# Kernel optimization log

Measured on AMD Instinct MI355X. Metric: run time of the kernel, lower is better.

## Reference

```python
import jax, jax.numpy as jnp
import numpy as np

B, S, D = 8, 4096, 256
NUM_WINDOW = 8
WIN = S // NUM_WINDOW          # 512
H = 2                          # num_heads
K = D                          # key_dim = d_model per source
DFF = 1024
LN_EPS = 1e-3                  # keras LayerNormalization default epsilon


def _layer_norm(x, g, b):
    mu = jnp.mean(x, axis=-1, keepdims=True)
    var = jnp.mean(jnp.square(x - mu), axis=-1, keepdims=True)
    return (x - mu) * jax.lax.rsqrt(var + LN_EPS) * g + b


def setup_inputs() -> dict:
    key = jax.random.key(0)
    ks = jax.random.split(key, 12)
    s = 0.02
    inp = {
        "x": jax.random.normal(ks[0], (B, S, D), dtype=jnp.float32),
        # MHA projections (keras MultiHeadAttention layout)
        "Wq": jax.random.normal(ks[1], (D, H, K), dtype=jnp.float32) * s,
        "bq": jnp.zeros((H, K), dtype=jnp.float32),
        "Wk": jax.random.normal(ks[2], (D, H, K), dtype=jnp.float32) * s,
        "bk": jnp.zeros((H, K), dtype=jnp.float32),
        "Wv": jax.random.normal(ks[3], (D, H, K), dtype=jnp.float32) * s,
        "bv": jnp.zeros((H, K), dtype=jnp.float32),
        "Wo": jax.random.normal(ks[4], (H, K, D), dtype=jnp.float32) * s,
        "bo": jnp.zeros((D,), dtype=jnp.float32),
        "ln1_g": jnp.ones((D,), dtype=jnp.float32),
        "ln1_b": jnp.zeros((D,), dtype=jnp.float32),
        # FeedForward
        "W1": jax.random.normal(ks[5], (D, DFF), dtype=jnp.float32) * s,
        "b1": jnp.zeros((DFF,), dtype=jnp.float32),
        "W2": jax.random.normal(ks[6], (DFF, D), dtype=jnp.float32) * s,
        "b2": jnp.zeros((D,), dtype=jnp.float32),
        "ln2_g": jnp.ones((D,), dtype=jnp.float32),
        "ln2_b": jnp.zeros((D,), dtype=jnp.float32),
    }
    return inp


def reference(x, Wq, bq, Wk, bk, Wv, bv, Wo, bo, ln1_g, ln1_b,
              W1, b1, W2, b2, ln2_g, ln2_b):
    # --- Localized self-attention: block-diagonal over NUM_WINDOW windows ---
    xw = x.reshape(B, NUM_WINDOW, WIN, D)               # [b, w, s, d]
    q = jnp.einsum('bwsd,dhk->bwshk', xw, Wq) + bq      # [b, w, s, h, k]
    k = jnp.einsum('bwsd,dhk->bwshk', xw, Wk) + bk
    v = jnp.einsum('bwsd,dhk->bwshk', xw, Wv) + bv
    scores = jnp.einsum('bwshk,bwthk->bwhst', q, k) / jnp.sqrt(
        jnp.asarray(K, dtype=x.dtype))                  # [b, w, h, s, t]
    attn = jax.nn.softmax(scores, axis=-1)
    ctx = jnp.einsum('bwhst,bwthk->bwshk', attn, v)     # [b, w, s, h, k]
    attn_out = jnp.einsum('bwshk,hkd->bwsd', ctx, Wo) + bo
    attn_out = attn_out.reshape(B, S, D)                # concat over windows
    x = _layer_norm(x + attn_out, ln1_g, ln1_b)
    # --- FeedForward (dropout inactive at inference) ---
    h = jax.nn.relu(x @ W1 + b1)
    ff = h @ W2 + b2
    return _layer_norm(x + ff, ln2_g, ln2_b)
```

## Files before the change

kernel.cpp:

```cpp
#include <hip/hip_runtime.h>

typedef unsigned short u16;
typedef short short8 __attribute__((ext_vector_type(8)));
typedef float f32x4 __attribute__((ext_vector_type(4)));

#define AS1C const __attribute__((address_space(1))) void*
#define AS3P __attribute__((address_space(3))) void*

__device__ __forceinline__ u16 f2b(float f) {
  unsigned u = __float_as_uint(f);
  return (u16)((u + 0x7fffu + ((u >> 16) & 1u)) >> 16);
}
__device__ __forceinline__ float b2f(u16 h) {
  return __uint_as_float((unsigned)h << 16);
}

#define BB 8
#define SS 4096
#define DD 256
#define MTOK (BB*SS)

#define OFF_WQKVT  ((size_t)0)
#define OFF_WOT    ((size_t)786432)
#define OFF_W1T    ((size_t)1048576)
#define OFF_W2T    ((size_t)1572864)
#define OFF_BQKV   ((size_t)2097152)
#define OFF_XB     ((size_t)2103296)
#define OFF_QKV    ((size_t)18880512)
#define OFF_YB     ((size_t)52434944)
#define OFF_HB     ((size_t)69212160)
#define OFF_VT     ((size_t)119543808)
#define OFF_CTX    ((size_t)153098240)
#define OFF_S      ((size_t)186652672)

__global__ __launch_bounds__(256) void cast_x_kernel(const float* __restrict__ x,
                                                     u16* __restrict__ xb) {
  size_t i = ((size_t)blockIdx.x * 256 + threadIdx.x) * 4;
  float4 v = *(const float4*)(x + i);
  ushort4 o;
  o.x = f2b(v.x); o.y = f2b(v.y); o.z = f2b(v.z); o.w = f2b(v.w);
  *(ushort4*)(xb + i) = o;
}

__global__ __launch_bounds__(256) void prep_w_kernel(
    const float* __restrict__ Wq, const float* __restrict__ Wk, const float* __restrict__ Wv,
    const float* __restrict__ Wo, const float* __restrict__ W1, const float* __restrict__ W2,
    const float* __restrict__ bq, const float* __restrict__ bk, const float* __restrict__ bv,
    u16* __restrict__ wqkvt, u16* __restrict__ wot, u16* __restrict__ w1t,
    u16* __restrict__ w2t, float* __restrict__ bqkv)
{
  for (int i = blockIdx.x * 256 + threadIdx.x; i < 1050112; i += 1024 * 256) {
    if (i < 393216) {
      int n = i >> 8, d = i & 255;
      const float* W = (n < 512) ? Wq : (n < 1024) ? Wk : Wv;
      int nn = n & 511;
      wqkvt[i] = f2b(W[d * 512 + nn]);
    } else if (i < 524288) {
      int j = i - 393216;
      int dout = j >> 9, hk = j & 511;
      wot[j] = f2b(Wo[hk * 256 + dout]);
    } else if (i < 786432) {
      int j = i - 524288;
      int f = j >> 8, d = j & 255;
      w1t[j] = f2b(W1[d * 1024 + f]);
    } else if (i < 1048576) {
      int j = i - 786432;
      int d = j >> 10, f = j & 1023;
      w2t[j] = f2b(W2[f * 256 + d]);
    } else {
      int n = i - 1048576;
      bqkv[n] = (n < 512) ? bq[n] : (n < 1024) ? bk[n - 512] : bv[n - 1024];
    }
  }
}

__global__ __launch_bounds__(256) void gemm_nres(
    const u16* __restrict__ A, const u16* __restrict__ BT,
    const float* __restrict__ bias, u16* __restrict__ C,
    u16* __restrict__ vt, int N, int vbase, int relu)
{
  __shared__ __align__(16) u16 lds[32768];
  const int tid = threadIdx.x, lane = tid & 63, wid = tid >> 6;
  const int ln = lane & 15, quad = lane >> 4;
  const int pn = blockIdx.x >> 6;
  const int mg = blockIdx.x & 63;
  const int wm = (wid >> 1) << 5;
  const int wn = (wid & 1) << 6;
  const long mbase = (long)mg << 9;
  const int nb = pn << 7;
  const u16* Bp = BT + (size_t)nb * 256;
  const u16* Ap = A + (size_t)mbase * 256;

#pragma unroll
  for (int p = 0; p < 16; p++) {
    const int s = p * 256 + tid;
    const int row = s >> 5, pc = s & 31;
    const int c = pc ^ (row & 31);
    __builtin_amdgcn_global_load_lds(
        (AS1C)(Bp + (size_t)row * 256 + c * 8), (AS3P)(lds + s * 8), 16, 0, 0);
  }
  __syncthreads();
  short8 breg[4][8];
#pragma unroll
  for (int j = 0; j < 4; j++) {
    const int row = wn + j * 16 + ln;
#pragma unroll
    for (int ks = 0; ks < 8; ks++)
      breg[j][ks] = *(const short8*)(lds + row * 256 + (((ks << 2) + quad) ^ (row & 31)) * 8);
  }
  __syncthreads();

#pragma unroll
  for (int p = 0; p < 8; p++) {
    const int s = p * 256 + tid;
    const int row = s >> 5, pc = s & 31;
    const int c = pc ^ (row & 31);
    __builtin_amdgcn_global_load_lds(
        (AS1C)(Ap + (size_t)row * 256 + c * 8), (AS3P)(lds + s * 8), 16, 0, 0);
  }

  for (int it = 0; it < 8; it++) {
    const int cur = it & 1;
    const u16* Ab = lds + cur * 16384;
    __syncthreads();
    if (it + 1 < 8) {
      const u16* An = Ap + (size_t)(it + 1) * 64 * 256;
      u16* Ax = lds + (cur ^ 1) * 16384;
#pragma unroll
      for (int p = 0; p < 8; p++) {
        const int s = p * 256 + tid;
        const int row = s >> 5, pc = s & 31;
        const int c = pc ^ (row & 31);
        __builtin_amdgcn_global_load_lds(
            (AS1C)(An + (size_t)row * 256 + c * 8), (AS3P)(Ax + s * 8), 16, 0, 0);
      }
    }
    f32x4 acc[2][4];
#pragma unroll
    for (int i = 0; i < 2; i++)
#pragma unroll
      for (int j = 0; j < 4; j++) acc[i][j] = (f32x4){0.f, 0.f, 0.f, 0.f};
    const int r0 = wm + ln, r1 = wm + 16 + ln;
#pragma unroll
    for (int ks = 0; ks < 8; ks++) {
      const short8 a0 = *(const short8*)(Ab + r0 * 256 + (((ks << 2) + quad) ^ (r0 & 31)) * 8);
      const short8 a1 = *(const short8*)(Ab + r1 * 256 + (((ks << 2) + quad) ^ (r1 & 31)) * 8);
#pragma unroll
      for (int j = 0; j < 4; j++) {
        acc[0][j] = __builtin_amdgcn_mfma_f32_16x16x32_bf16(breg[j][ks], a0, acc[0][j], 0, 0, 0);
        acc[1][j] = __builtin_amdgcn_mfma_f32_16x16x32_bf16(breg[j][ks], a1, acc[1][j], 0, 0, 0);
      }
    }
    const long mrow0 = mbase + it * 64;
    if (nb < vbase) {
#pragma unroll
      for (int i = 0; i < 2; i++) {
        const long m = mrow0 + wm + i * 16 + ln;
#pragma unroll
        for (int j = 0; j < 4; j++) {
          const int n0 = nb + wn + j * 16 + quad * 4;
          f32x4 v = acc[i][j];
          const float4 b4 = *(const float4*)(bias + n0);
          v[0] += b4.x; v[1] += b4.y; v[2] += b4.z; v[3] += b4.w;
          if (relu) {
#pragma unroll
            for (int r = 0; r < 4; r++) v[r] = fmaxf(v[r], 0.f);
          }
          ushort4 ob;
          ob.x = f2b(v[0]); ob.y = f2b(v[1]); ob.z = f2b(v[2]); ob.w = f2b(v[3]);
          *(ushort4*)(C + (size_t)m * N + n0) = ob;
        }
      }
    } else {
#pragma unroll
      for (int i = 0; i < 2; i++) {
        const long m = mrow0 + wm + i * 16 + ln;
        const int bw = (int)(m >> 9), t = (int)(m & 511);
#pragma unroll
        for (int j = 0; j < 4; j++) {
          const int n0 = nb + wn + j * 16 + quad * 4;
          const int h = (n0 - vbase) >> 8, k0 = (n0 - vbase) & 255;
          u16* vp = vt + (size_t)(bw * 2 + h) * 131072 + (size_t)k0 * 512 + t;
          const float4 b4 = *(const float4*)(bias + n0);
          vp[0]    = f2b(acc[i][j][0] + b4.x);
          vp[512]  = f2b(acc[i][j][1] + b4.y);
          vp[1024] = f2b(acc[i][j][2] + b4.z);
          vp[1536] = f2b(acc[i][j][3] + b4.w);
        }
      }
    }
  }
}

__global__ __launch_bounds__(512) void bgemm_qk(const u16* __restrict__ qkv,
                                                u16* __restrict__ S)
{
  __shared__ __align__(16) u16 As[64 * 32];
  __shared__ __align__(16) u16 Bs[512 * 32];
  __shared__ float red1[8][64], red2[8][64];
  const int tid = threadIdx.x, lane = tid & 63, wid = tid >> 6;
  const int ln = lane & 15, quad = lane >> 4;
  const int bat = blockIdx.x & 127, mt = blockIdx.x >> 7;
  const int bw = bat >> 1, h = bat & 1;
  const u16* Qb = qkv + (size_t)bw * 786432 + (size_t)h * 256 + (size_t)(mt * 64) * 1536;
  const u16* Kb = qkv + (size_t)bw * 786432 + 512 + (size_t)h * 256;
  u16* Sb = S + (size_t)bat * 262144 + (size_t)(mt * 64) * 512;
  const int wn = wid * 64;

  f32x4 acc[4][4];
#pragma unroll
  for (int i = 0; i < 4; i++)
#pragma unroll
    for (int j = 0; j < 4; j++) acc[i][j] = (f32x4){0.f, 0.f, 0.f, 0.f};

  for (int kt = 0; kt < 256; kt += 32) {
    if (tid < 256) {
      const int row = tid >> 2, c = tid & 3;
      __builtin_amdgcn_global_load_lds(
          (AS1C)(Qb + (size_t)row * 1536 + kt + c * 8), (AS3P)(As + tid * 8), 16, 0, 0);
    }
#pragma unroll
    for (int p = 0; p < 4; p++) {
      const int s = p * 512 + tid;
      const int row = s >> 2, c = s & 3;
      __builtin_amdgcn_global_load_lds(
          (AS1C)(Kb + (size_t)row * 1536 + kt + c * 8), (AS3P)(Bs + s * 8), 16, 0, 0);
    }
    __syncthreads();
    short8 a[4], b[4];
#pragma unroll
    for (int i = 0; i < 4; i++) a[i] = *(const short8*)(As + (i * 16 + ln) * 32 + quad * 8);
#pragma unroll
    for (int j = 0; j < 4; j++) b[j] = *(const short8*)(Bs + (wn + j * 16 + ln) * 32 + quad * 8);
#pragma unroll
    for (int i = 0; i < 4; i++)
#pragma unroll
      for (int j = 0; j < 4; j++)
        acc[i][j] = __builtin_amdgcn_mfma_f32_16x16x32_bf16(b[j], a[i], acc[i][j], 0, 0, 0);
    __syncthreads();
  }

  float rowmax[4];
#pragma unroll
  for (int i = 0; i < 4; i++) {
    float m = -1e30f;
#pragma unroll
    for (int j = 0; j < 4; j++)
#pragma unroll
      for (int r = 0; r < 4; r++) m = fmaxf(m, acc[i][j][r]);
    m = fmaxf(m, __shfl_xor(m, 16));
    m = fmaxf(m, __shfl_xor(m, 32));
    if (quad == 0) red1[wid][i * 16 + ln] = m;
    rowmax[i] = m;
  }
  __syncthreads();
#pragma unroll
  for (int i = 0; i < 4; i++) {
    float m = -1e30f;
#pragma unroll
    for (int w = 0; w < 8; w++) m = fmaxf(m, red1[w][i * 16 + ln]);
    rowmax[i] = m;
  }
  float rowsum[4];
#pragma unroll
  for (int i = 0; i < 4; i++) {
    float s = 0.f;
#pragma unroll
    for (int j = 0; j < 4; j++)
#pragma unroll
      for (int r = 0; r < 4; r++) {
        const float e = __expf((acc[i][j][r] - rowmax[i]) * 0.0625f);
        acc[i][j][r] = e; s += e;
      }
    s += __shfl_xor(s, 16);
    s += __shfl_xor(s, 32);
    if (quad == 0) red2[wid][i * 16 + ln] = s;
  }
  __syncthreads();
#pragma unroll
  for (int i = 0; i < 4; i++) {
    float s = 0.f;
#pragma unroll
    for (int w = 0; w < 8; w++) s += red2[w][i * 16 + ln];
    rowsum[i] = 1.f / s;
  }
#pragma unroll
  for (int i = 0; i < 4; i++) {
    const size_t roff = (size_t)(i * 16 + ln) * 512;
#pragma unroll
    for (int j = 0; j < 4; j++) {
      const int n0 = wn + j * 16 + quad * 4;
      ushort4 ob;
      ob.x = f2b(acc[i][j][0] * rowsum[i]);
      ob.y = f2b(acc[i][j][1] * rowsum[i]);
      ob.z = f2b(acc[i][j][2] * rowsum[i]);
      ob.w = f2b(acc[i][j][3] * rowsum[i]);
      *(ushort4*)(Sb + roff + n0) = ob;
    }
  }
}

#define GSTAGE(Sptr, Gptr, ld)                                                     \
  __builtin_amdgcn_global_load_lds(                                                \
      (AS1C)((Gptr) + (size_t)rr * (ld) + kt2 + skk),                              \
      (AS3P)((Sptr) + (size_t)(i * 64 + wid * 16) * 32), 16, 0, 0)

__global__ __launch_bounds__(256) void bgemm(
    const u16* __restrict__ A, long sAbw, long sAh, int lda,
    const u16* __restrict__ B, long sBbw, long sBh, int ldb,
    u16* __restrict__ C, long sCbw, long sCh, int ldc,
    int K, int Ntiles)
{
  __shared__ __align__(16) u16 As[2][128 * 32];
  __shared__ __align__(16) u16 Bs[2][128 * 32];
  const int tid = threadIdx.x, lane = tid & 63, wid = tid >> 6;
  const int ln = lane & 15, quad = lane >> 4;
  const int blk = blockIdx.x & 127;
  const int rem = blockIdx.x >> 7;
  const int mt = rem / Ntiles, nt = rem % Ntiles;
  const int bw = blk >> 1, h = blk & 1;
  const u16* Ab = A + (size_t)bw * sAbw + (size_t)h * sAh + (size_t)mt * 128 * lda;
  const u16* Bp = B + (size_t)bw * sBbw + (size_t)h * sBh + (size_t)nt * 128 * ldb;
  u16*       Cp = C + (size_t)bw * sCbw + (size_t)h * sCh + (size_t)mt * 128 * ldc + nt * 128;
  const int srow = lane >> 2;
  const int skk  = (lane & 3) << 3;
  const int wm = (wid >> 1) << 6, wn = (wid & 1) << 6;

  f32x4 acc[4][4];
#pragma unroll
  for (int i = 0; i < 4; i++)
#pragma unroll
    for (int j = 0; j < 4; j++) acc[i][j] = (f32x4){0.f, 0.f, 0.f, 0.f};

  {
    const int kt2 = 0;
#pragma unroll
    for (int i = 0; i < 2; i++) {
      const int rr = i * 64 + wid * 16 + srow;
      GSTAGE(As[0], Ab, lda);
      GSTAGE(Bs[0], Bp, ldb);
    }
  }
  int cur = 0;
  for (int kt = 0; kt < K; kt += 32, cur ^= 1) {
    __syncthreads();
    if (kt + 32 < K) {
      const int kt2 = kt + 32;
#pragma unroll
      for (int i = 0; i < 2; i++) {
        const int rr = i * 64 + wid * 16 + srow;
        GSTAGE(As[cur ^ 1], Ab, lda);
        GSTAGE(Bs[cur ^ 1], Bp, ldb);
      }
    }
    short8 a[4], b[4];
#pragma unroll
    for (int i = 0; i < 4; i++) a[i] = *(const short8*)(As[cur] + (wm + i * 16 + ln) * 32 + quad * 8);
#pragma unroll
    for (int j = 0; j < 4; j++) b[j] = *(const short8*)(Bs[cur] + (wn + j * 16 + ln) * 32 + quad * 8);
#pragma unroll
    for (int i = 0; i < 4; i++)
#pragma unroll
      for (int j = 0; j < 4; j++)
        acc[i][j] = __builtin_amdgcn_mfma_f32_16x16x32_bf16(b[j], a[i], acc[i][j], 0, 0, 0);
  }

#pragma unroll
  for (int i = 0; i < 4; i++) {
    const int m = wm + i * 16 + ln;
#pragma unroll
    for (int j = 0; j < 4; j++) {
      const int n0 = wn + j * 16 + quad * 4;
      const f32x4 v = acc[i][j];
      ushort4 ob;
      ob.x = f2b(v[0]); ob.y = f2b(v[1]); ob.z = f2b(v[2]); ob.w = f2b(v[3]);
      *(ushort4*)(Cp + (size_t)m * ldc + n0) = ob;
    }
  }
}

__global__ __launch_bounds__(256) void gemm_ln(
    const u16* __restrict__ A, const u16* __restrict__ BT,
    const float* __restrict__ bias, const u16* __restrict__ residb,
    const float* __restrict__ g, const float* __restrict__ beta,
    float* __restrict__ yout, u16* __restrict__ ybout, int K)
{
  __shared__ __align__(16) u16 As[64 * 32];
  __shared__ __align__(16) u16 Bs[256 * 32];
  __shared__ float redS[4][64], redQ[4][64];
  const int tid = threadIdx.x, lane = tid & 63, wid = tid >> 6;
  const int ln = lane & 15, quad = lane >> 4;
  const long bm = (long)blockIdx.x * 64;
  const int wn = wid * 64;
  const u16* Ab = A + (size_t)bm * K;

  f32x4 acc[4][4];
#pragma unroll
  for (int i = 0; i < 4; i++)
#pragma unroll
    for (int j = 0; j < 4; j++) acc[i][j] = (f32x4){0.f, 0.f, 0.f, 0.f};

  for (int kt = 0; kt < K; kt += 32) {
    {
      const int row = tid >> 2, c = tid & 3;
      __builtin_amdgcn_global_load_lds(
          (AS1C)(Ab + (size_t)row * K + kt + c * 8), (AS3P)(As + tid * 8), 16, 0, 0);
    }
#pragma unroll
    for (int p = 0; p < 4; p++) {
      const int s = p * 256 + tid;
      const int row = s >> 2, c = s & 3;
      __builtin_amdgcn_global_load_lds(
          (AS1C)(BT + (size_t)row * K + kt + c * 8), (AS3P)(Bs + s * 8), 16, 0, 0);
    }
    __syncthreads();
    short8 a[4], b[4];
#pragma unroll
    for (int i = 0; i < 4; i++) a[i] = *(const short8*)(As + (i * 16 + ln) * 32 + quad * 8);
#pragma unroll
    for (int j = 0; j < 4; j++) b[j] = *(const short8*)(Bs + (wn + j * 16 + ln) * 32 + quad * 8);
#pragma unroll
    for (int i = 0; i < 4; i++)
#pragma unroll
      for (int j = 0; j < 4; j++)
        acc[i][j] = __builtin_amdgcn_mfma_f32_16x16x32_bf16(b[j], a[i], acc[i][j], 0, 0, 0);
    __syncthreads();
  }

#pragma unroll
  for (int i = 0; i < 4; i++) {
    const long gm = bm + i * 16 + ln;
    float s = 0.f, q = 0.f;
#pragma unroll
    for (int j = 0; j < 4; j++) {
      const int n0 = wn + j * 16 + quad * 4;
      const float4 b4 = *(const float4*)(bias + n0);
      const ushort4 r4 = *(const ushort4*)(residb + (size_t)gm * 256 + n0);
      acc[i][j][0] += b4.x + b2f(r4.x);
      acc[i][j][1] += b4.y + b2f(r4.y);
      acc[i][j][2] += b4.z + b2f(r4.z);
      acc[i][j][3] += b4.w + b2f(r4.w);
#pragma unroll
      for (int r = 0; r < 4; r++) { s += acc[i][j][r]; q += acc[i][j][r] * acc[i][j][r]; }
    }
    s += __shfl_xor(s, 16); s += __shfl_xor(s, 32);
    q += __shfl_xor(q, 16); q += __shfl_xor(q, 32);
    if (quad == 0) { redS[wid][i * 16 + ln] = s; redQ[wid][i * 16 + ln] = q; }
  }
  __syncthreads();
#pragma unroll
  for (int i = 0; i < 4; i++) {
    const long gm = bm + i * 16 + ln;
    float s = 0.f, q = 0.f;
#pragma unroll
    for (int w = 0; w < 4; w++) { s += redS[w][i * 16 + ln]; q += redQ[w][i * 16 + ln]; }
    const float mu = s * (1.f / 256.f);
    const float inv = rsqrtf(q * (1.f / 256.f) - mu * mu + 1e-3f);
#pragma unroll
    for (int j = 0; j < 4; j++) {
      const int n0 = wn + j * 16 + quad * 4;
      const float4 gg = *(const float4*)(g + n0);
      const float4 bb = *(const float4*)(beta + n0);
      float o0 = (acc[i][j][0] - mu) * inv * gg.x + bb.x;
      float o1 = (acc[i][j][1] - mu) * inv * gg.y + bb.y;
      float o2 = (acc[i][j][2] - mu) * inv * gg.z + bb.z;
      float o3 = (acc[i][j][3] - mu) * inv * gg.w + bb.w;
      const size_t off = (size_t)gm * 256 + n0;
      if (yout) {
        float4 o4; o4.x = o0; o4.y = o1; o4.z = o2; o4.w = o3;
        *(float4*)(yout + off) = o4;
      }
      if (ybout) {
        ushort4 ob;
        ob.x = f2b(o0); ob.y = f2b(o1); ob.z = f2b(o2); ob.w = f2b(o3);
        *(ushort4*)(ybout + off) = ob;
      }
    }
  }
}

extern "C" void kernel_launch(void* const* d_in, const int* in_sizes, int n_in,
                              void* d_out, int out_size, void* d_ws, size_t ws_size,
                              hipStream_t stream) {
  (void)in_sizes; (void)n_in; (void)out_size; (void)ws_size;
  const float* x    = (const float*)d_in[0];
  const float* Wq   = (const float*)d_in[1];
  const float* bq   = (const float*)d_in[2];
  const float* Wk   = (const float*)d_in[3];
  const float* bk   = (const float*)d_in[4];
  const float* Wv   = (const float*)d_in[5];
  const float* bv   = (const float*)d_in[6];
  const float* Wo   = (const float*)d_in[7];
  const float* bo   = (const float*)d_in[8];
  const float* ln1g = (const float*)d_in[9];
  const float* ln1b = (const float*)d_in[10];
  const float* W1   = (const float*)d_in[11];
  const float* b1   = (const float*)d_in[12];
  const float* W2   = (const float*)d_in[13];
  const float* b2   = (const float*)d_in[14];
  const float* ln2g = (const float*)d_in[15];
  const float* ln2b = (const float*)d_in[16];
  float* out = (float*)d_out;

  char* ws = (char*)d_ws;
  u16*   WQKVT = (u16*)(ws + OFF_WQKVT);
  u16*   WOT   = (u16*)(ws + OFF_WOT);
  u16*   W1T   = (u16*)(ws + OFF_W1T);
  u16*   W2T   = (u16*)(ws + OFF_W2T);
  float* BQKV  = (float*)(ws + OFF_BQKV);
  u16*   XB    = (u16*)(ws + OFF_XB);
  u16*   QKV   = (u16*)(ws + OFF_QKV);
  u16*   YB    = (u16*)(ws + OFF_YB);
  u16*   HB    = (u16*)(ws + OFF_HB);
  u16*   VT    = (u16*)(ws + OFF_VT);
  u16*   CTX   = (u16*)(ws + OFF_CTX);
  u16*   S     = (u16*)(ws + OFF_S);

  cast_x_kernel<<<8192, 256, 0, stream>>>(x, XB);
  prep_w_kernel<<<1024, 256, 0, stream>>>(Wq, Wk, Wv, Wo, W1, W2, bq, bk, bv,
                                          WQKVT, WOT, W1T, W2T, BQKV);
  gemm_nres<<<768, 256, 0, stream>>>(XB, WQKVT, BQKV, QKV, VT, 1536, 1024, 0);
  bgemm_qk<<<1024, 512, 0, stream>>>(QKV, S);
  bgemm<<<1024, 256, 0, stream>>>(S,   524288, 262144, 512,
                                  VT,  262144, 131072, 512,
                                  CTX, 262144, 256, 512,
                                  512, 2);
  gemm_ln<<<512, 256, 0, stream>>>(CTX, WOT, bo, XB, ln1g, ln1b, nullptr, YB, 512);
  gemm_nres<<<512, 256, 0, stream>>>(YB, W1T, b1, HB, nullptr, 1024, 1 << 30, 1);
  gemm_ln<<<512, 256, 0, stream>>>(HB, W2T, b2, YB, ln2g, ln2b, out, nullptr, 1024);
}
```

Before: 373.2 us.

## Fuse QK softmax and PV into one attention kernel; retile projection GEMM

Replaces the separate score GEMM with softmax and the batched PV GEMM with a single attn_fused kernel. It keeps the softmax probabilities on chip, stages them per 64-key chunk into LDS, and multiplies by V tiles loaded into LDS. This removes the round trip of the 512x512 score matrix through global memory. The projection GEMM is also retiled to 64-wide N tiles and 32-row M steps with half the LDS, and the launch counts are kept consistent. The cost is that only one wave writes P per chunk, with extra barriers, and the smaller GEMM tiles get less operand reuse.

```diff
diff --git a/kernel.cpp b/kernel.cpp
--- a/kernel.cpp
+++ b/kernel.cpp
@@ -31,7 +31,6 @@
 #define OFF_HB     ((size_t)69212160)
 #define OFF_VT     ((size_t)119543808)
 #define OFF_CTX    ((size_t)153098240)
-#define OFF_S      ((size_t)186652672)
 
 __global__ __launch_bounds__(256) void cast_x_kernel(const float* __restrict__ x,
                                                      u16* __restrict__ xb) {
@@ -79,20 +78,20 @@
     const float* __restrict__ bias, u16* __restrict__ C,
     u16* __restrict__ vt, int N, int vbase, int relu)
 {
-  __shared__ __align__(16) u16 lds[32768];
+  __shared__ __align__(16) u16 lds[16384];
   const int tid = threadIdx.x, lane = tid & 63, wid = tid >> 6;
   const int ln = lane & 15, quad = lane >> 4;
-  const int pn = blockIdx.x >> 6;
-  const int mg = blockIdx.x & 63;
-  const int wm = (wid >> 1) << 5;
-  const int wn = (wid & 1) << 6;
-  const long mbase = (long)mg << 9;
-  const int nb = pn << 7;
+  const int pn = blockIdx.x >> 5;
+  const int mg = blockIdx.x & 31;
+  const int wno = (wid >> 1) << 5;
+  const int wmo = (wid & 1) << 4;
+  const long mbase = (long)mg << 10;
+  const int nb = pn << 6;
   const u16* Bp = BT + (size_t)nb * 256;
   const u16* Ap = A + (size_t)mbase * 256;
 
 #pragma unroll
-  for (int p = 0; p < 16; p++) {
+  for (int p = 0; p < 8; p++) {
     const int s = p * 256 + tid;
     const int row = s >> 5, pc = s & 31;
     const int c = pc ^ (row & 31);
@@ -100,10 +99,10 @@
         (AS1C)(Bp + (size_t)row * 256 + c * 8), (AS3P)(lds + s * 8), 16, 0, 0);
   }
   __syncthreads();
-  short8 breg[4][8];
-#pragma unroll
-  for (int j = 0; j < 4; j++) {
-    const int row = wn + j * 16 + ln;
+  short8 breg[2][8];
+#pragma unroll
+  for (int j = 0; j < 2; j++) {
+    const int row = wno + j * 16 + ln;
 #pragma unroll
     for (int ks = 0; ks < 8; ks++)
       breg[j][ks] = *(const short8*)(lds + row * 256 + (((ks << 2) + quad) ^ (row & 31)) * 8);
@@ -111,7 +110,7 @@
   __syncthreads();
 
 #pragma unroll
-  for (int p = 0; p < 8; p++) {
+  for (int p = 0; p < 4; p++) {
     const int s = p * 256 + tid;
     const int row = s >> 5, pc = s & 31;
     const int c = pc ^ (row & 31);
@@ -119,15 +118,15 @@
         (AS1C)(Ap + (size_t)row * 256 + c * 8), (AS3P)(lds + s * 8), 16, 0, 0);
   }
 
-  for (int it = 0; it < 8; it++) {
+  for (int it = 0; it < 32; it++) {
     const int cur = it & 1;
-    const u16* Ab = lds + cur * 16384;
-    __syncthreads();
-    if (it + 1 < 8) {
-      const u16* An = Ap + (size_t)(it + 1) * 64 * 256;
-      u16* Ax = lds + (cur ^ 1) * 16384;
-#pragma unroll
-      for (int p = 0; p < 8; p++) {
+    const u16* Ab = lds + cur * 8192;
+    __syncthreads();
+    if (it + 1 < 32) {
+      const u16* An = Ap + (size_t)(it + 1) * 32 * 256;
+      u16* Ax = lds + (cur ^ 1) * 8192;
+#pragma unroll
+      for (int p = 0; p < 4; p++) {
         const int s = p * 256 + tid;
         const int row = s >> 5, pc = s & 31;
         const int c = pc ^ (row & 31);
@@ -135,77 +134,65 @@
             (AS1C)(An + (size_t)row * 256 + c * 8), (AS3P)(Ax + s * 8), 16, 0, 0);
       }
     }
-    f32x4 acc[2][4];
-#pragma unroll
-    for (int i = 0; i < 2; i++)
-#pragma unroll
-      for (int j = 0; j < 4; j++) acc[i][j] = (f32x4){0.f, 0.f, 0.f, 0.f};
-    const int r0 = wm + ln, r1 = wm + 16 + ln;
+    f32x4 acc[2];
+    acc[0] = (f32x4){0.f, 0.f, 0.f, 0.f};
+    acc[1] = (f32x4){0.f, 0.f, 0.f, 0.f};
+    const int r0 = wmo + ln;
 #pragma unroll
     for (int ks = 0; ks < 8; ks++) {
       const short8 a0 = *(const short8*)(Ab + r0 * 256 + (((ks << 2) + quad) ^ (r0 & 31)) * 8);
-      const short8 a1 = *(const short8*)(Ab + r1 * 256 + (((ks << 2) + quad) ^ (r1 & 31)) * 8);
-#pragma unroll
-      for (int j = 0; j < 4; j++) {
-        acc[0][j] = __builtin_amdgcn_mfma_f32_16x16x32_bf16(breg[j][ks], a0, acc[0][j], 0, 0, 0);
-        acc[1][j] = __builtin_amdgcn_mfma_f32_16x16x32_bf16(breg[j][ks], a1, acc[1][j], 0, 0, 0);
-      }
-    }
-    const long mrow0 = mbase + it * 64;
+      acc[0] = __builtin_amdgcn_mfma_f32_16x16x32_bf16(breg[0][ks], a0, acc[0], 0, 0, 0);
+      acc[1] = __builtin_amdgcn_mfma_f32_16x16x32_bf16(breg[1][ks], a0, acc[1], 0, 0, 0);
+    }
+    const long m = mbase + it * 32 + wmo + ln;
     if (nb < vbase) {
 #pragma unroll
-      for (int i = 0; i < 2; i++) {
-        const long m = mrow0 + wm + i * 16 + ln;
-#pragma unroll
-        for (int j = 0; j < 4; j++) {
-          const int n0 = nb + wn + j * 16 + quad * 4;
-          f32x4 v = acc[i][j];
-          const float4 b4 = *(const float4*)(bias + n0);
-          v[0] += b4.x; v[1] += b4.y; v[2] += b4.z; v[3] += b4.w;
-          if (relu) {
-#pragma unroll
-            for (int r = 0; r < 4; r++) v[r] = fmaxf(v[r], 0.f);
-          }
-          ushort4 ob;
-          ob.x = f2b(v[0]); ob.y = f2b(v[1]); ob.z = f2b(v[2]); ob.w = f2b(v[3]);
-          *(ushort4*)(C + (size_t)m * N + n0) = ob;
+      for (int j = 0; j < 2; j++) {
+        const int n0 = nb + wno + j * 16 + quad * 4;
+        f32x4 v = acc[j];
+        const float4 b4 = *(const float4*)(bias + n0);
+        v[0] += b4.x; v[1] += b4.y; v[2] += b4.z; v[3] += b4.w;
+        if (relu) {
+#pragma unroll
+          for (int r = 0; r < 4; r++) v[r] = fmaxf(v[r], 0.f);
         }
+        ushort4 ob;
+        ob.x = f2b(v[0]); ob.y = f2b(v[1]); ob.z = f2b(v[2]); ob.w = f2b(v[3]);
+        *(ushort4*)(C + (size_t)m * N + n0) = ob;
       }
     } else {
-#pragma unroll
-      for (int i = 0; i < 2; i++) {
-        const long m = mrow0 + wm + i * 16 + ln;
-        const int bw = (int)(m >> 9), t = (int)(m & 511);
-#pragma unroll
-        for (int j = 0; j < 4; j++) {
-          const int n0 = nb + wn + j * 16 + quad * 4;
-          const int h = (n0 - vbase) >> 8, k0 = (n0 - vbase) & 255;
-          u16* vp = vt + (size_t)(bw * 2 + h) * 131072 + (size_t)k0 * 512 + t;
-          const float4 b4 = *(const float4*)(bias + n0);
-          vp[0]    = f2b(acc[i][j][0] + b4.x);
-          vp[512]  = f2b(acc[i][j][1] + b4.y);
-          vp[1024] = f2b(acc[i][j][2] + b4.z);
-          vp[1536] = f2b(acc[i][j][3] + b4.w);
-        }
-      }
-    }
-  }
-}
-
-__global__ __launch_bounds__(512) void bgemm_qk(const u16* __restrict__ qkv,
-                                                u16* __restrict__ S)
+      const int bw = (int)(m >> 9), t = (int)(m & 511);
+#pragma unroll
+      for (int j = 0; j < 2; j++) {
+        const int n0 = nb + wno + j * 16 + quad * 4;
+        const int rel = n0 - vbase;
+        const int h = rel >> 8, k0 = rel & 255;
+        u16* vp = vt + (size_t)(bw * 2 + h) * 131072 + (size_t)k0 * 512 + t;
+        const float4 b4 = *(const float4*)(bias + n0);
+        vp[0]    = f2b(acc[j][0] + b4.x);
+        vp[512]  = f2b(acc[j][1] + b4.y);
+        vp[1024] = f2b(acc[j][2] + b4.z);
+        vp[1536] = f2b(acc[j][3] + b4.w);
+      }
+    }
+  }
+}
+
+__global__ __launch_bounds__(512) void attn_fused(const u16* __restrict__ qkv,
+                                                  const u16* __restrict__ vt,
+                                                  u16* __restrict__ ctx)
 {
-  __shared__ __align__(16) u16 As[64 * 32];
-  __shared__ __align__(16) u16 Bs[512 * 32];
-  __shared__ float red1[8][64], red2[8][64];
+  __shared__ __align__(16) u16 lds[20992];
   const int tid = threadIdx.x, lane = tid & 63, wid = tid >> 6;
   const int ln = lane & 15, quad = lane >> 4;
   const int bat = blockIdx.x & 127, mt = blockIdx.x >> 7;
   const int bw = bat >> 1, h = bat & 1;
   const u16* Qb = qkv + (size_t)bw * 786432 + (size_t)h * 256 + (size_t)(mt * 64) * 1536;
   const u16* Kb = qkv + (size_t)bw * 786432 + 512 + (size_t)h * 256;
-  u16* Sb = S + (size_t)bat * 262144 + (size_t)(mt * 64) * 512;
+  const u16* Vb = vt + (size_t)bat * 131072;
   const int wn = wid * 64;
+  float* red1 = (float*)(lds + 18432);
+  float* red2 = red1 + 512;
 
   f32x4 acc[4][4];
 #pragma unroll
@@ -217,21 +204,21 @@
     if (tid < 256) {
       const int row = tid >> 2, c = tid & 3;
       __builtin_amdgcn_global_load_lds(
-          (AS1C)(Qb + (size_t)row * 1536 + kt + c * 8), (AS3P)(As + tid * 8), 16, 0, 0);
+          (AS1C)(Qb + (size_t)row * 1536 + kt + c * 8), (AS3P)(lds + tid * 8), 16, 0, 0);
     }
 #pragma unroll
     for (int p = 0; p < 4; p++) {
       const int s = p * 512 + tid;
       const int row = s >> 2, c = s & 3;
       __builtin_amdgcn_global_load_lds(
-          (AS1C)(Kb + (size_t)row * 1536 + kt + c * 8), (AS3P)(Bs + s * 8), 16, 0, 0);
+          (AS1C)(Kb + (size_t)row * 1536 + kt + c * 8), (AS3P)(lds + 2048 + s * 8), 16, 0, 0);
     }
     __syncthreads();
     short8 a[4], b[4];
 #pragma unroll
-    for (int i = 0; i < 4; i++) a[i] = *(const short8*)(As + (i * 16 + ln) * 32 + quad * 8);
-#pragma unroll
-    for (int j = 0; j < 4; j++) b[j] = *(const short8*)(Bs + (wn + j * 16 + ln) * 32 + quad * 8);
+    for (int i = 0; i < 4; i++) a[i] = *(const short8*)(lds + (i * 16 + ln) * 32 + quad * 8);
+#pragma unroll
+    for (int j = 0; j < 4; j++) b[j] = *(const short8*)(lds + 2048 + (wn + j * 16 + ln) * 32 + quad * 8);
 #pragma unroll
     for (int i = 0; i < 4; i++)
 #pragma unroll
@@ -240,7 +227,7 @@
     __syncthreads();
   }
 
-  float rowmax[4];
+  float rowmax[4], rowsum[4];
 #pragma unroll
   for (int i = 0; i < 4; i++) {
     float m = -1e30f;
@@ -250,18 +237,16 @@
       for (int r = 0; r < 4; r++) m = fmaxf(m, acc[i][j][r]);
     m = fmaxf(m, __shfl_xor(m, 16));
     m = fmaxf(m, __shfl_xor(m, 32));
-    if (quad == 0) red1[wid][i * 16 + ln] = m;
+    if (quad == 0) red1[wid * 64 + i * 16 + ln] = m;
+  }
+  __syncthreads();
+#pragma unroll
+  for (int i = 0; i < 4; i++) {
+    float m = -1e30f;
+#pragma unroll
+    for (int w = 0; w < 8; w++) m = fmaxf(m, red1[w * 64 + i * 16 + ln]);
     rowmax[i] = m;
   }
-  __syncthreads();
-#pragma unroll
-  for (int i = 0; i < 4; i++) {
-    float m = -1e30f;
-#pragma unroll
-    for (int w = 0; w < 8; w++) m = fmaxf(m, red1[w][i * 16 + ln]);
-    rowmax[i] = m;
-  }
-  float rowsum[4];
 #pragma unroll
   for (int i = 0; i < 4; i++) {
     float s = 0.f;
@@ -274,107 +259,79 @@
       }
     s += __shfl_xor(s, 16);
     s += __shfl_xor(s, 32);
-    if (quad == 0) red2[wid][i * 16 + ln] = s;
+    if (quad == 0) red2[wid * 64 + i * 16 + ln] = s;
   }
   __syncthreads();
 #pragma unroll
   for (int i = 0; i < 4; i++) {
     float s = 0.f;
 #pragma unroll
-    for (int w = 0; w < 8; w++) s += red2[w][i * 16 + ln];
+    for (int w = 0; w < 8; w++) s += red2[w * 64 + i * 16 + ln];
     rowsum[i] = 1.f / s;
   }
-#pragma unroll
-  for (int i = 0; i < 4; i++) {
-    const size_t roff = (size_t)(i * 16 + ln) * 512;
-#pragma unroll
-    for (int j = 0; j < 4; j++) {
-      const int n0 = wn + j * 16 + quad * 4;
+
+  u16* Pb = lds;
+  u16* Vc = lds + 4608;
+  const int wno = wid * 32;
+  f32x4 o[4][2];
+#pragma unroll
+  for (int i = 0; i < 4; i++) {
+    o[i][0] = (f32x4){0.f, 0.f, 0.f, 0.f};
+    o[i][1] = (f32x4){0.f, 0.f, 0.f, 0.f};
+  }
+
+  for (int c = 0; c < 8; c++) {
+    __syncthreads();
+    if (wid == c) {
+#pragma unroll
+      for (int i = 0; i < 4; i++)
+#pragma unroll
+        for (int j = 0; j < 4; j++) {
+          ushort4 pb;
+          pb.x = f2b(acc[i][j][0] * rowsum[i]);
+          pb.y = f2b(acc[i][j][1] * rowsum[i]);
+          pb.z = f2b(acc[i][j][2] * rowsum[i]);
+          pb.w = f2b(acc[i][j][3] * rowsum[i]);
+          *(ushort4*)(Pb + (i * 16 + ln) * 72 + j * 16 + quad * 4) = pb;
+        }
+    }
+#pragma unroll
+    for (int p = 0; p < 4; p++) {
+      const int s = p * 512 + tid;
+      const int row = s >> 3, pc = s & 7;
+      const int cc = pc ^ (row & 7);
+      __builtin_amdgcn_global_load_lds(
+          (AS1C)(Vb + (size_t)row * 512 + c * 64 + cc * 8), (AS3P)(Vc + s * 8), 16, 0, 0);
+    }
+    __syncthreads();
+#pragma unroll
+    for (int ks = 0; ks < 2; ks++) {
+      short8 ap[4];
+#pragma unroll
+      for (int i = 0; i < 4; i++)
+        ap[i] = *(const short8*)(Pb + (i * 16 + ln) * 72 + ks * 32 + quad * 8);
+#pragma unroll
+      for (int j = 0; j < 2; j++) {
+        const int kV = wno + j * 16 + ln;
+        const short8 bv = *(const short8*)(Vc + kV * 64 + (((ks << 2) + quad) ^ (kV & 7)) * 8);
+#pragma unroll
+        for (int i = 0; i < 4; i++)
+          o[i][j] = __builtin_amdgcn_mfma_f32_16x16x32_bf16(bv, ap[i], o[i][j], 0, 0, 0);
+      }
+    }
+  }
+
+  const size_t tokr0 = (size_t)bw * 512 + mt * 64;
+#pragma unroll
+  for (int i = 0; i < 4; i++) {
+    const size_t row = tokr0 + i * 16 + ln;
+#pragma unroll
+    for (int j = 0; j < 2; j++) {
+      const int col = h * 256 + wno + j * 16 + quad * 4;
       ushort4 ob;
-      ob.x = f2b(acc[i][j][0] * rowsum[i]);
-      ob.y = f2b(acc[i][j][1] * rowsum[i]);
-      ob.z = f2b(acc[i][j][2] * rowsum[i]);
-      ob.w = f2b(acc[i][j][3] * rowsum[i]);
-      *(ushort4*)(Sb + roff + n0) = ob;
-    }
-  }
-}
-
-#define GSTAGE(Sptr, Gptr, ld)                                                     \
-  __builtin_amdgcn_global_load_lds(                                                \
-      (AS1C)((Gptr) + (size_t)rr * (ld) + kt2 + skk),                              \
-      (AS3P)((Sptr) + (size_t)(i * 64 + wid * 16) * 32), 16, 0, 0)
-
-__global__ __launch_bounds__(256) void bgemm(
-    const u16* __restrict__ A, long sAbw, long sAh, int lda,
-    const u16* __restrict__ B, long sBbw, long sBh, int ldb,
-    u16* __restrict__ C, long sCbw, long sCh, int ldc,
-    int K, int Ntiles)
-{
-  __shared__ __align__(16) u16 As[2][128 * 32];
-  __shared__ __align__(16) u16 Bs[2][128 * 32];
-  const int tid = threadIdx.x, lane = tid & 63, wid = tid >> 6;
-  const int ln = lane & 15, quad = lane >> 4;
-  const int blk = blockIdx.x & 127;
-  const int rem = blockIdx.x >> 7;
-  const int mt = rem / Ntiles, nt = rem % Ntiles;
-  const int bw = blk >> 1, h = blk & 1;
-  const u16* Ab = A + (size_t)bw * sAbw + (size_t)h * sAh + (size_t)mt * 128 * lda;
-  const u16* Bp = B + (size_t)bw * sBbw + (size_t)h * sBh + (size_t)nt * 128 * ldb;
-  u16*       Cp = C + (size_t)bw * sCbw + (size_t)h * sCh + (size_t)mt * 128 * ldc + nt * 128;
-  const int srow = lane >> 2;
-  const int skk  = (lane & 3) << 3;
-  const int wm = (wid >> 1) << 6, wn = (wid & 1) << 6;
-
-  f32x4 acc[4][4];
-#pragma unroll
-  for (int i = 0; i < 4; i++)
-#pragma unroll
-    for (int j = 0; j < 4; j++) acc[i][j] = (f32x4){0.f, 0.f, 0.f, 0.f};
-
-  {
-    const int kt2 = 0;
-#pragma unroll
-    for (int i = 0; i < 2; i++) {
-      const int rr = i * 64 + wid * 16 + srow;
-      GSTAGE(As[0], Ab, lda);
-      GSTAGE(Bs[0], Bp, ldb);
-    }
-  }
-  int cur = 0;
-  for (int kt = 0; kt < K; kt += 32, cur ^= 1) {
-    __syncthreads();
-    if (kt + 32 < K) {
-      const int kt2 = kt + 32;
-#pragma unroll
-      for (int i = 0; i < 2; i++) {
-        const int rr = i * 64 + wid * 16 + srow;
-        GSTAGE(As[cur ^ 1], Ab, lda);
-        GSTAGE(Bs[cur ^ 1], Bp, ldb);
-      }
-    }
-    short8 a[4], b[4];
-#pragma unroll
-    for (int i = 0; i < 4; i++) a[i] = *(const short8*)(As[cur] + (wm + i * 16 + ln) * 32 + quad * 8);
-#pragma unroll
-    for (int j = 0; j < 4; j++) b[j] = *(const short8*)(Bs[cur] + (wn + j * 16 + ln) * 32 + quad * 8);
-#pragma unroll
-    for (int i = 0; i < 4; i++)
-#pragma unroll
-      for (int j = 0; j < 4; j++)
-        acc[i][j] = __builtin_amdgcn_mfma_f32_16x16x32_bf16(b[j], a[i], acc[i][j], 0, 0, 0);
-  }
-
-#pragma unroll
-  for (int i = 0; i < 4; i++) {
-    const int m = wm + i * 16 + ln;
-#pragma unroll
-    for (int j = 0; j < 4; j++) {
-      const int n0 = wn + j * 16 + quad * 4;
-      const f32x4 v = acc[i][j];
-      ushort4 ob;
-      ob.x = f2b(v[0]); ob.y = f2b(v[1]); ob.z = f2b(v[2]); ob.w = f2b(v[3]);
-      *(ushort4*)(Cp + (size_t)m * ldc + n0) = ob;
+      ob.x = f2b(o[i][j][0]); ob.y = f2b(o[i][j][1]);
+      ob.z = f2b(o[i][j][2]); ob.w = f2b(o[i][j][3]);
+      *(ushort4*)(ctx + row * 512 + col) = ob;
     }
   }
 }
@@ -514,17 +471,12 @@
   u16*   HB    = (u16*)(ws + OFF_HB);
   u16*   VT    = (u16*)(ws + OFF_VT);
   u16*   CTX   = (u16*)(ws + OFF_CTX);
-  u16*   S     = (u16*)(ws + OFF_S);
 
   cast_x_kernel<<<8192, 256, 0, stream>>>(x, XB);
   prep_w_kernel<<<1024, 256, 0, stream>>>(Wq, Wk, Wv, Wo, W1, W2, bq, bk, bv,
                                           WQKVT, WOT, W1T, W2T, BQKV);
   gemm_nres<<<768, 256, 0, stream>>>(XB, WQKVT, BQKV, QKV, VT, 1536, 1024, 0);
-  bgemm_qk<<<1024, 512, 0, stream>>>(QKV, S);
-  bgemm<<<1024, 256, 0, stream>>>(S,   524288, 262144, 512,
-                                  VT,  262144, 131072, 512,
-                                  CTX, 262144, 256, 512,
-                                  512, 2);
+  attn_fused<<<1024, 512, 0, stream>>>(QKV, VT, CTX);
   gemm_ln<<<512, 256, 0, stream>>>(CTX, WOT, bo, XB, ln1g, ln1b, nullptr, YB, 512);
   gemm_nres<<<512, 256, 0, stream>>>(YB, W1T, b1, HB, nullptr, 1024, 1 << 30, 1);
   gemm_ln<<<512, 256, 0, stream>>>(HB, W2T, b2, YB, ln2g, ln2b, out, nullptr, 1024);
```

Result: no change. 368.5 us (-1.3%).
